# Optimization experiments

Measured on AMD Instinct MI355X. Metric: run time of the kernel, lower is better.

The kernel has to match this reference:

```python
import jax, jax.numpy as jnp
import numpy as np

EPS = 1e-5

def lrelu(x):
    return jnp.where(x > 0, x, 0.2 * x)

def bn(x, g, b, ch_axis=1):
    # BatchNorm in training-mode math (batch statistics), affine
    axes = tuple(i for i in range(x.ndim) if i != ch_axis)
    m = x.mean(axes, keepdims=True)
    v = x.var(axes, keepdims=True)
    shp = [1] * x.ndim; shp[ch_axis] = -1
    return g.reshape(shp) * (x - m) / jnp.sqrt(v + EPS) + b.reshape(shp)

def get_graph_feature(x, idx):
    # x: (B,C,N), idx: (B,N,k) -> edge features (B,2C,N,k) = [neighbor - center, center]
    xt = jnp.transpose(x, (0, 2, 1))                      # (B,N,C)
    nb = jax.vmap(lambda pts, i: pts[i])(xt, idx)         # gather: (B,N,k,C)
    center = jnp.broadcast_to(xt[:, :, None, :], nb.shape)
    edge = jnp.concatenate([nb - center, center], axis=-1)  # (B,N,k,2C)
    return jnp.transpose(edge, (0, 3, 1, 2))              # (B,2C,N,k)

def setup_inputs() -> dict:
    key = jax.random.key(0)
    ks = jax.random.split(key, 12)
    B, N, K = 4, 2048, 20
    def w(k, o, c, s=0.05):
        return jax.random.normal(k, (o, c), jnp.float32) * s
    inp = {}
    inp["x"] = jax.random.normal(ks[0], (B, N, 3), jnp.float32)
    inp["start_neighs"] = jax.random.randint(ks[1], (B, N, K), 0, N)
    dims = [(6, 64), (128, 128), (256, 256), (512, 512)]
    for i, (ci, co) in enumerate(dims):
        inp["w%d" % i] = w(ks[2 + i], co, ci)
        inp["g%d" % i] = jnp.ones((co,), jnp.float32)
        inp["b%d" % i] = jnp.zeros((co,), jnp.float32)
    inp["w4"] = w(ks[6], 1024, 960)
    inp["g4"] = jnp.ones((1024,), jnp.float32); inp["b4"] = jnp.zeros((1024,), jnp.float32)
    inp["lw1"] = w(ks[7], 1024, 2048)
    inp["g6"] = jnp.ones((1024,), jnp.float32); inp["b6"] = jnp.zeros((1024,), jnp.float32)
    inp["lw2"] = w(ks[8], 512, 1024); inp["lb2"] = jnp.zeros((512,), jnp.float32)
    inp["g7"] = jnp.ones((512,), jnp.float32); inp["b7"] = jnp.zeros((512,), jnp.float32)
    inp["lw3"] = w(ks[9], 256, 512); inp["lb3"] = jnp.zeros((256,), jnp.float32)
    return inp

def reference(x, start_neighs,
              w0, g0, b0, w1, g1, b1, w2, g2, b2, w3, g3, b3,
              w4, g4, b4, lw1, g6, b6, lw2, lb2, g7, b7, lw3, lb3):
    # forward_per_point
    xt = jnp.transpose(x, (0, 2, 1))                      # (B,3,N)
    h = get_graph_feature(xt, start_neighs)               # (B,6,N,k)
    outs = []
    for (w, g, b) in ((w0, g0, b0), (w1, g1, b1), (w2, g2, b2), (w3, g3, b3)):
        if outs:  # only_true_neighs=True -> reuse start_neighs
            h = get_graph_feature(outs[-1], start_neighs)
        h = lrelu(bn(jnp.einsum('oc,bcnk->bonk', w, h), g, b))  # 1x1 Conv2d + BN + LeakyReLU
        outs.append(h.max(axis=-1))                       # max over k neighbors -> (B,C,N)
    cat = jnp.concatenate(outs, axis=1)                   # (B,960,N)
    feats = lrelu(bn(jnp.einsum('oc,bcn->bon', w4, cat), g4, b4))  # (B,1024,N)
    # aggregate_all_points (dropout p=0 -> identity)
    z = jnp.concatenate([feats.max(-1), feats.mean(-1)], axis=1)   # (B,2048)
    z = lrelu(bn(z @ lw1.T, g6, b6))
    z = lrelu(bn(z @ lw2.T + lb2, g7, b7))
    z = z @ lw3.T + lb3                                   # (B,256)
    # forward returns (aggregated.squeeze(-1), features_per_point.transpose(1,2)) = (z, (B,1024,N))
    return z, feats
```

## Files before the change

### kernel.cpp

```cpp
#include <hip/hip_runtime.h>
#include <cstddef>
#include <cstdint>

#define EPSBN 1e-5f
constexpr int B_ = 4, N_ = 2048, K_ = 20;

typedef __attribute__((ext_vector_type(8))) _Float16 half8v;
typedef __attribute__((ext_vector_type(4))) float f32x4;
typedef const __attribute__((address_space(1))) unsigned int* gas_t;
typedef __attribute__((address_space(3))) unsigned int* las_t;

__device__ __forceinline__ void swz_batch(int B, int& b, int& local) {
    b = (B & 7) >> 1;
    local = ((B >> 3) << 1) | (B & 1);
}


__device__ __forceinline__ void prep_conv(const float* __restrict__ W, _Float16* __restrict__ W2h,
                                          int O, int C, int i) {
    int o = i / C, c = i - o * C;
    float a = W[o * 2 * C + c];
    float d = W[o * 2 * C + C + c] - a;
    W2h[(size_t)o * C + c] = (_Float16)a;
    W2h[(size_t)(O + o) * C + c] = (_Float16)d;
}

__global__ void k_prep_all(const float* __restrict__ w1, const float* __restrict__ w2,
                           const float* __restrict__ w3, const float* __restrict__ w4,
                           _Float16* __restrict__ W2h1, _Float16* __restrict__ W2h2,
                           _Float16* __restrict__ W2h3, _Float16* __restrict__ w4h) {
    int i = blockIdx.x * 256 + threadIdx.x;
    if (i < 8192) { prep_conv(w1, W2h1, 128, 64, i); return; }
    i -= 8192;
    if (i < 32768) { prep_conv(w2, W2h2, 256, 128, i); return; }
    i -= 32768;
    if (i < 131072) { prep_conv(w3, W2h3, 512, 256, i); return; }
    i -= 131072;
    if (i < 983040) w4h[i] = (_Float16)w4[i];
}

template<bool STATS>
__global__ __launch_bounds__(256, 3)
void k_gemm(const _Float16* __restrict__ A, int sa,
            const _Float16* __restrict__ Bw, int K,
            _Float16* __restrict__ outp, int so,
            float* __restrict__ psum, float* __restrict__ psq) {
    __shared__ __align__(16) _Float16 Als[128 * 64];
    __shared__ __align__(16) _Float16 Bls[128 * 64];
    const int tid = threadIdx.x, lane = tid & 63, w = tid >> 6;
    int bsw, lsw;
    swz_batch(blockIdx.x, bsw, lsw);
    const int m0 = (bsw * 16 + lsw) * 128;
    const int n0 = blockIdx.y * 128;
    const int wr = (w >> 1) * 64, wc = (w & 1) * 64;

    f32x4 acc[4][4];
#pragma unroll
    for (int i = 0; i < 4; ++i)
#pragma unroll
        for (int j = 0; j < 4; ++j) acc[i][j] = (f32x4){0.f, 0.f, 0.f, 0.f};

    int srow[4], scol[4];
#pragma unroll
    for (int j = 0; j < 4; ++j) {
        int idx = w * 256 + j * 64 + lane;
        srow[j] = idx >> 3;
        scol[j] = ((idx & 7) ^ (srow[j] & 7)) * 8;
    }
    int aoff[4][2], boff[4][2];
#pragma unroll
    for (int i = 0; i < 4; ++i) {
        int ra = wr + i * 16 + (lane & 15);
        int rb = wc + i * 16 + (lane & 15);
#pragma unroll
        for (int t = 0; t < 2; ++t) {
            aoff[i][t] = ra * 64 + ((((lane >> 4) + t * 4) ^ (ra & 7)) * 8);
            boff[i][t] = rb * 64 + ((((lane >> 4) + t * 4) ^ (rb & 7)) * 8);
        }
    }

    for (int c0 = 0; c0 < K; c0 += 64) {
#pragma unroll
        for (int j = 0; j < 4; ++j) {
            const _Float16* ga = &A[(size_t)(m0 + srow[j]) * sa + c0 + scol[j]];
            const _Float16* gb = &Bw[(size_t)(n0 + srow[j]) * K + c0 + scol[j]];
            __builtin_amdgcn_global_load_lds((gas_t)(const void*)ga,
                                             (las_t)(void*)&Als[(w * 256 + j * 64) * 8], 16, 0, 0);
            __builtin_amdgcn_global_load_lds((gas_t)(const void*)gb,
                                             (las_t)(void*)&Bls[(w * 256 + j * 64) * 8], 16, 0, 0);
        }
        __syncthreads();
#pragma unroll
        for (int t = 0; t < 2; ++t) {
            half8v a[4], b[4];
#pragma unroll
            for (int i = 0; i < 4; ++i) {
                a[i] = *(const half8v*)&Als[aoff[i][t]];
                b[i] = *(const half8v*)&Bls[boff[i][t]];
            }
#pragma unroll
            for (int i = 0; i < 4; ++i)
#pragma unroll
                for (int j = 0; j < 4; ++j)
                    acc[i][j] = __builtin_amdgcn_mfma_f32_16x16x32_f16(a[i], b[j], acc[i][j], 0, 0, 0);
        }
        __syncthreads();
    }
#pragma unroll
    for (int i = 0; i < 4; ++i)
#pragma unroll
        for (int j = 0; j < 4; ++j)
#pragma unroll
            for (int e = 0; e < 4; ++e) {
                int row = m0 + wr + i * 16 + (lane >> 4) * 4 + e;
                int col = n0 + wc + j * 16 + (lane & 15);
                outp[(size_t)row * so + col] = (_Float16)acc[i][j][e];
            }
    if constexpr (STATS) {
        int slice = blockIdx.x & 63;
#pragma unroll
        for (int j = 0; j < 4; ++j) {
            float s = 0.f, q = 0.f;
#pragma unroll
            for (int i = 0; i < 4; ++i)
#pragma unroll
                for (int e = 0; e < 4; ++e) {
                    float v = acc[i][j][e];
                    s += v; q += v * v;
                }
            s += __shfl_xor(s, 16); s += __shfl_xor(s, 32);
            q += __shfl_xor(q, 16); q += __shfl_xor(q, 32);
            if ((lane >> 4) == 0) {
                int col = n0 + wc + j * 16 + lane;
                atomicAdd(&psum[slice * 1024 + col], s);
                atomicAdd(&psq[slice * 1024 + col], q);
            }
        }
    }
}

__global__ __launch_bounds__(256)
void k_gather0(const float* __restrict__ x, const float* __restrict__ w0,
               const int* __restrict__ nidx, const float* __restrict__ g,
               _Float16* __restrict__ exth,
               float* __restrict__ psum, float* __restrict__ psq) {
    constexpr int O = 64, VPT = 8, P = 32;
    __shared__ float s_red[P * O];
    __shared__ float q_red[P * O];
    const int tid = threadIdx.x;
    const int pl = tid / VPT, v = tid % VPT;
    int bsw, local;
    swz_batch(blockIdx.x, bsw, local);
    const int bbase = bsw * N_;
    const int p = bbase + local * P + pl;
    float wa[8][3], wd[8][3], sg[8];
#pragma unroll
    for (int e = 0; e < 8; ++e) {
        int o = v * 8 + e;
        float a0 = w0[o * 6], a1 = w0[o * 6 + 1], a2 = w0[o * 6 + 2];
        wa[e][0] = a0; wa[e][1] = a1; wa[e][2] = a2;
        wd[e][0] = w0[o * 6 + 3] - a0;
        wd[e][1] = w0[o * 6 + 4] - a1;
        wd[e][2] = w0[o * 6 + 5] - a2;
        sg[e] = (g[o] >= 0.f) ? 1.f : -1.f;
    }
    float mx[8], sm[8], sq[8];
#pragma unroll
    for (int e = 0; e < 8; ++e) { mx[e] = -3.4e38f; sm[e] = 0.f; sq[e] = 0.f; }
    const int* np = nidx + p * K_;
#pragma unroll 4
    for (int k = 0; k < K_; ++k) {
        int j = bbase + np[k];
        float x0 = x[j * 3], x1 = x[j * 3 + 1], x2 = x[j * 3 + 2];
#pragma unroll
        for (int e = 0; e < 8; ++e) {
            float f = wa[e][0] * x0 + wa[e][1] * x1 + wa[e][2] * x2;
            mx[e] = fmaxf(mx[e], f * sg[e]);
            sm[e] += f;
            sq[e] += f * f;
        }
    }
    float xp0 = x[p * 3], xp1 = x[p * 3 + 1], xp2 = x[p * 3 + 2];
    const float Kf = (float)K_;
    half8v exo;
#pragma unroll
    for (int e = 0; e < 8; ++e) {
        float zf = wd[e][0] * xp0 + wd[e][1] * xp1 + wd[e][2] * xp2;
        exo[e] = (_Float16)(sg[e] * mx[e] + zf);
        s_red[pl * O + v * 8 + e] = sm[e] + Kf * zf;
        q_red[pl * O + v * 8 + e] = sq[e] + 2.f * zf * sm[e] + Kf * zf * zf;
    }
    *(half8v*)&exth[(size_t)p * O + v * 8] = exo;
    __syncthreads();
    int slice = blockIdx.x & 63;
    for (int ch = tid; ch < O; ch += 256) {
        float s = 0.f, q = 0.f;
#pragma unroll
        for (int pp = 0; pp < P; ++pp) { s += s_red[pp * O + ch]; q += q_red[pp * O + ch]; }
        atomicAdd(&psum[slice * 1024 + ch], s);
        atomicAdd(&psq[slice * 1024 + ch], q);
    }
}

template<int O>
__global__ __launch_bounds__(256)
void k_gather(const _Float16* __restrict__ Z, const int* __restrict__ nidx,
              const float* __restrict__ g,
              _Float16* __restrict__ exth,
              float* __restrict__ psum, float* __restrict__ psq) {
    constexpr int VPT = O / 8, P = 256 / VPT;
    __shared__ float s_red[P * O];
    __shared__ float q_red[P * O];
    const int tid = threadIdx.x;
    const int pl = tid / VPT, v = tid % VPT;
    int bsw, local;
    swz_batch(blockIdx.x, bsw, local);
    const int bbase = bsw * N_;
    const int p = bbase + local * P + pl;
    float sg[8];
#pragma unroll
    for (int e = 0; e < 8; ++e) sg[e] = (g[v * 8 + e] >= 0.f) ? 1.f : -1.f;
    float mx[8], sm[8], sq[8];
#pragma unroll
    for (int e = 0; e < 8; ++e) { mx[e] = -3.4e38f; sm[e] = 0.f; sq[e] = 0.f; }
    const int* np = nidx + p * K_;
#pragma unroll 4
    for (int k = 0; k < K_; ++k) {
        int j = np[k];
        half8v z = *(const half8v*)&Z[(size_t)(bbase + j) * (2 * O) + v * 8];
#pragma unroll
        for (int e = 0; e < 8; ++e) {
            float f = (float)z[e];
            mx[e] = fmaxf(mx[e], f * sg[e]);
            sm[e] += f;
            sq[e] += f * f;
        }
    }
    half8v zd = *(const half8v*)&Z[(size_t)p * (2 * O) + O + v * 8];
    const float Kf = (float)K_;
    half8v exo;
#pragma unroll
    for (int e = 0; e < 8; ++e) {
        float zf = (float)zd[e];
        exo[e] = (_Float16)(sg[e] * mx[e] + zf);
        s_red[pl * O + v * 8 + e] = sm[e] + Kf * zf;
        q_red[pl * O + v * 8 + e] = sq[e] + 2.f * zf * sm[e] + Kf * zf * zf;
    }
    *(half8v*)&exth[(size_t)p * O + v * 8] = exo;
    __syncthreads();
    int slice = blockIdx.x & 63;
    for (int ch = tid; ch < O; ch += 256) {
        float s = 0.f, q = 0.f;
#pragma unroll
        for (int pp = 0; pp < P; ++pp) { s += s_red[pp * O + ch]; q += q_red[pp * O + ch]; }
        atomicAdd(&psum[slice * 1024 + ch], s);
        atomicAdd(&psq[slice * 1024 + ch], q);
    }
}

__global__ void k_finalize_sl(const float* __restrict__ psum, const float* __restrict__ psq,
                              const float* __restrict__ g, const float* __restrict__ b,
                              float cntInv, int O,
                              float* __restrict__ scale, float* __restrict__ shift) {
    int o = blockIdx.x * 256 + threadIdx.x;
    if (o >= O) return;
    float s = 0.f, q = 0.f;
    for (int i = 0; i < 64; ++i) { s += psum[i * 1024 + o]; q += psq[i * 1024 + o]; }
    float m = s * cntInv;
    float v = q * cntInv - m * m;
    float sc = g[o] * rsqrtf(fmaxf(v, 0.f) + EPSBN);
    scale[o] = sc;
    shift[o] = b[o] - m * sc;
}

template<int O>
__global__ void k_bn_apply(const _Float16* __restrict__ exth,
                           const float* __restrict__ scale, const float* __restrict__ shift,
                           _Float16* __restrict__ cath, int coff) {
    constexpr int PPB = 2048 / O;
    int bsw, local;
    swz_batch(blockIdx.x, bsw, local);
    const int pt_base = bsw * N_ + local * PPB;
    int tid = threadIdx.x;
    int pt = pt_base + (tid * 8) / O;
    int v8 = (tid * 8) & (O - 1);
    half8v hx = *(const half8v*)&exth[(size_t)pt * O + v8];
    half8v r;
#pragma unroll
    for (int e = 0; e < 8; ++e) {
        int o = v8 + e;
        float y = scale[o] * (float)hx[e] + shift[o];
        y = y > 0.f ? y : 0.2f * y;
        r[e] = (_Float16)y;
    }
    *(half8v*)&cath[(size_t)pt * 960 + coff + v8] = r;
}

__global__ void k_feats_out(const _Float16* __restrict__ Y4, const float* __restrict__ scale,
                            const float* __restrict__ shift, float* __restrict__ fo,
                            float* __restrict__ pmax, float* __restrict__ psumn) {
    __shared__ float tile[32][33];
    int tx = threadIdx.x, ty = threadIdx.y;
    int b = blockIdx.z;
    int n0 = blockIdx.x * 32, c0 = blockIdx.y * 32;
#pragma unroll
    for (int i = 0; i < 4; ++i) {
        int n = n0 + ty + i * 8;
        int c = c0 + tx;
        float v = (float)Y4[((size_t)(b * N_ + n)) * 1024 + c];
        v = scale[c] * v + shift[c];
        v = v > 0.f ? v : 0.2f * v;
        tile[ty + i * 8][tx] = v;
    }
    __syncthreads();
#pragma unroll
    for (int i = 0; i < 4; ++i) {
        int c = c0 + ty + i * 8;
        int n = n0 + tx;
        float v2 = tile[tx][ty + i * 8];
        fo[((size_t)(b * 1024 + c)) * N_ + n] = v2;
        float mx = v2, s = v2;
#pragma unroll
        for (int d = 1; d < 32; d <<= 1) {
            mx = fmaxf(mx, __shfl_xor(mx, d));
            s += __shfl_xor(s, d);
        }
        if (tx == 0) {
            int bc = (b << 10) + c;
            pmax[(size_t)bc * 64 + blockIdx.x] = mx;
            psumn[(size_t)bc * 64 + blockIdx.x] = s;
        }
    }
}

__global__ void k_pool2(const float* __restrict__ pmax, const float* __restrict__ psumn,
                        float* __restrict__ z0) {
    int bc = blockIdx.x * 4 + (threadIdx.x >> 6);
    int lane = threadIdx.x & 63;
    float mx = pmax[(size_t)bc * 64 + lane];
    float s  = psumn[(size_t)bc * 64 + lane];
#pragma unroll
    for (int d = 1; d < 64; d <<= 1) {
        mx = fmaxf(mx, __shfl_xor(mx, d));
        s += __shfl_xor(s, d);
    }
    if (lane == 0) {
        int b = bc >> 10, c = bc & 1023;
        z0[b * 2048 + c] = mx;
        z0[b * 2048 + 1024 + c] = s * (1.f / N_);
    }
}

__global__ void k_fc(const float* __restrict__ zin, const float* __restrict__ W,
                     const float* __restrict__ bias,
                     const float* __restrict__ gg, const float* __restrict__ gb,
                     int C, int O, float* __restrict__ zout) {
    __shared__ float sh4[4];
    const int b = threadIdx.x >> 6;
    const int lane = threadIdx.x & 63;
    const int o = blockIdx.x;
    const float* wr = W + (size_t)o * C;
    const float* zr = zin + b * C;
    float s = 0.f;
    for (int c = lane * 4; c < C; c += 256) {
        const float4 wv = *(const float4*)&wr[c];
        const float4 zv = *(const float4*)&zr[c];
        s += wv.x * zv.x + wv.y * zv.y + wv.z * zv.z + wv.w * zv.w;
    }
    s += __shfl_xor(s, 1);
    s += __shfl_xor(s, 2);
    s += __shfl_xor(s, 4);
    s += __shfl_xor(s, 8);
    s += __shfl_xor(s, 16);
    s += __shfl_xor(s, 32);
    if (!gg) {
        if (lane == 0) zout[b * O + o] = s + (bias ? bias[o] : 0.f);
        return;
    }
    if (lane == 0) sh4[b] = s + (bias ? bias[o] : 0.f);
    __syncthreads();
    if (threadIdx.x == 0) {
        float v0 = sh4[0], v1 = sh4[1], v2 = sh4[2], v3 = sh4[3];
        float m = 0.25f * (v0 + v1 + v2 + v3);
        float d0 = v0 - m, d1 = v1 - m, d2 = v2 - m, d3 = v3 - m;
        float var = 0.25f * (d0 * d0 + d1 * d1 + d2 * d2 + d3 * d3);
        float sc = gg[o] * rsqrtf(var + EPSBN);
        float shv = gb[o];
        float r0 = sc * d0 + shv, r1 = sc * d1 + shv, r2 = sc * d2 + shv, r3 = sc * d3 + shv;
        zout[o]         = r0 > 0.f ? r0 : 0.2f * r0;
        zout[O + o]     = r1 > 0.f ? r1 : 0.2f * r1;
        zout[2 * O + o] = r2 > 0.f ? r2 : 0.2f * r2;
        zout[3 * O + o] = r3 > 0.f ? r3 : 0.2f * r3;
    }
}


extern "C" void kernel_launch(void* const* d_in, const int* in_sizes, int n_in,
                              void* d_out, int out_size, void* d_ws, size_t ws_size,
                              hipStream_t stream) {
    const float* x    = (const float*)d_in[0];
    const int*   nidx = (const int*)d_in[1];
    const float* w[5]  = {(const float*)d_in[2], (const float*)d_in[5], (const float*)d_in[8],
                          (const float*)d_in[11], (const float*)d_in[14]};
    const float* g[5]  = {(const float*)d_in[3], (const float*)d_in[6], (const float*)d_in[9],
                          (const float*)d_in[12], (const float*)d_in[15]};
    const float* bb[5] = {(const float*)d_in[4], (const float*)d_in[7], (const float*)d_in[10],
                          (const float*)d_in[13], (const float*)d_in[16]};
    const float* lw1 = (const float*)d_in[17];
    const float* g6  = (const float*)d_in[18];
    const float* b6  = (const float*)d_in[19];
    const float* lw2 = (const float*)d_in[20];
    const float* lb2 = (const float*)d_in[21];
    const float* g7  = (const float*)d_in[22];
    const float* b7  = (const float*)d_in[23];
    const float* lw3 = (const float*)d_in[24];
    const float* lb3 = (const float*)d_in[25];

    float* out = (float*)d_out;
    float* fo  = out + 1024;

    uint8_t* base8 = (uint8_t*)d_ws;
    size_t off = 0;
    auto alloc = [&](size_t bytes) -> void* {
        void* r = base8 + off;
        off += (bytes + 255) & ~(size_t)255;
        return r;
    };
    _Float16* cath = (_Float16*)alloc((size_t)B_ * N_ * 960 * 2);
    _Float16* Z    = (_Float16*)alloc((size_t)8192 * 1024 * 2);
    _Float16* exth = (_Float16*)alloc((size_t)8192 * 512 * 2);
    _Float16* Y4   = (_Float16*)alloc((size_t)8192 * 1024 * 2);
    _Float16* W2h1 = (_Float16*)alloc((size_t)256 * 64 * 2);
    _Float16* W2h2 = (_Float16*)alloc((size_t)512 * 128 * 2);
    _Float16* W2h3 = (_Float16*)alloc((size_t)1024 * 256 * 2);
    _Float16* w4h  = (_Float16*)alloc((size_t)1024 * 960 * 2);
    float* psumall = (float*)alloc((size_t)5 * 131072 * 4);
    float* pmax  = (float*)alloc((size_t)4096 * 64 * 4);
    float* psumn = (float*)alloc((size_t)4096 * 64 * 4);
    float* scalev= (float*)alloc(1024 * 4);
    float* shiftv= (float*)alloc(1024 * 4);
    float* z0    = (float*)alloc(8192 * 4);
    float* z1    = (float*)alloc(4096 * 4);
    float* z2    = (float*)alloc(2048 * 4);
    (void)ws_size; (void)in_sizes; (void)n_in; (void)out_size;

    auto psumR = [&](int r) { return psumall + (size_t)r * 131072; };
    auto psqR  = [&](int r) { return psumall + (size_t)r * 131072 + 65536; };

    hipMemsetAsync(psumall, 0, (size_t)5 * 131072 * 4, stream);
    k_prep_all<<<(8192 + 32768 + 131072 + 983040 + 255) / 256, 256, 0, stream>>>(
        w[1], w[2], w[3], w[4], W2h1, W2h2, W2h3, w4h);

    k_gather0<<<256, 256, 0, stream>>>(x, w[0], nidx, g[0], exth, psumR(0), psqR(0));
    k_finalize_sl<<<1, 256, 0, stream>>>(psumR(0), psqR(0), g[0], bb[0], 1.f / (B_ * N_ * K_),
                                         64, scalev, shiftv);
    k_bn_apply<64><<<256, 256, 0, stream>>>(exth, scalev, shiftv, cath, 0);

    struct LayerCfg { int coff_in, C, O, coff_out, li; const _Float16* Wh; };
    const LayerCfg L[3] = {
        { 0,   64,  128, 64,  1, W2h1 },
        { 64,  128, 256, 192, 2, W2h2 },
        { 192, 256, 512, 448, 3, W2h3 },
    };
    for (int i = 0; i < 3; ++i) {
        const LayerCfg& Lc = L[i];
        dim3 ggrid(64, (2 * Lc.O) / 128);
        k_gemm<false><<<ggrid, 256, 0, stream>>>(cath + Lc.coff_in, 960, Lc.Wh, Lc.C,
                                                 Z, 2 * Lc.O, nullptr, nullptr);
        if (Lc.O == 128) {
            k_gather<128><<<512, 256, 0, stream>>>(Z, nidx, g[Lc.li], exth, psumR(i + 1), psqR(i + 1));
            k_finalize_sl<<<1, 256, 0, stream>>>(psumR(i + 1), psqR(i + 1), g[Lc.li], bb[Lc.li],
                                                 1.f / (B_ * N_ * K_), 128, scalev, shiftv);
            k_bn_apply<128><<<512, 256, 0, stream>>>(exth, scalev, shiftv, cath, Lc.coff_out);
        } else if (Lc.O == 256) {
            k_gather<256><<<1024, 256, 0, stream>>>(Z, nidx, g[Lc.li], exth, psumR(i + 1), psqR(i + 1));
            k_finalize_sl<<<1, 256, 0, stream>>>(psumR(i + 1), psqR(i + 1), g[Lc.li], bb[Lc.li],
                                                 1.f / (B_ * N_ * K_), 256, scalev, shiftv);
            k_bn_apply<256><<<1024, 256, 0, stream>>>(exth, scalev, shiftv, cath, Lc.coff_out);
        } else {
            k_gather<512><<<2048, 256, 0, stream>>>(Z, nidx, g[Lc.li], exth, psumR(i + 1), psqR(i + 1));
            k_finalize_sl<<<2, 256, 0, stream>>>(psumR(i + 1), psqR(i + 1), g[Lc.li], bb[Lc.li],
                                                 1.f / (B_ * N_ * K_), 512, scalev, shiftv);
            k_bn_apply<512><<<2048, 256, 0, stream>>>(exth, scalev, shiftv, cath, Lc.coff_out);
        }
    }

    k_gemm<true><<<dim3(64, 8), 256, 0, stream>>>(cath, 960, w4h, 960, Y4, 1024, psumR(4), psqR(4));
    k_finalize_sl<<<4, 256, 0, stream>>>(psumR(4), psqR(4), g[4], bb[4], 1.f / (B_ * N_), 1024,
                                         scalev, shiftv);
    k_feats_out<<<dim3(64, 32, 4), dim3(32, 8), 0, stream>>>(Y4, scalev, shiftv, fo, pmax, psumn);
    k_pool2<<<1024, 256, 0, stream>>>(pmax, psumn, z0);

    k_fc<<<1024, 256, 0, stream>>>(z0, lw1, nullptr, g6, b6, 2048, 1024, z1);
    k_fc<<<512, 256, 0, stream>>>(z1, lw2, lb2, g7, b7, 1024, 512, z2);
    k_fc<<<256, 256, 0, stream>>>(z2, lw3, lb3, nullptr, nullptr, 512, 256, out);
}
```

Before: 168.6 us.

## Fuse BN-apply and LeakyReLU into GEMM A-tile load, drop concat buffer

Removes the separate k_bn_apply kernels and the concatenated cath buffer. Each GEMM now reads the raw per-layer max-pooled outputs, applies BN scale/shift and LeakyReLU in registers, and writes the result to LDS. The final 960-channel GEMM picks among four source buffers per K-chunk. This drops three kernel launches and an extra read/write pass over the activations. The cost is that A loads now go through registers instead of direct global-to-LDS transfers, and the normalisation is recomputed for every N-tile block.

```diff
diff --git a/kernel.cpp b/kernel.cpp
--- a/kernel.cpp
+++ b/kernel.cpp
@@ -41,7 +41,12 @@
 
 template<bool STATS>
 __global__ __launch_bounds__(256, 3)
-void k_gemm(const _Float16* __restrict__ A, int sa,
+void k_gemm(const _Float16* __restrict__ A0, const _Float16* __restrict__ A1,
+            const _Float16* __restrict__ A2, const _Float16* __restrict__ A3,
+            int t1, int t2, int t3,
+            int c1, int c2, int c3,
+            int s0, int s1, int s2, int s3,
+            const float* __restrict__ scale, const float* __restrict__ shift,
             const _Float16* __restrict__ Bw, int K,
             _Float16* __restrict__ outp, int so,
             float* __restrict__ psum, float* __restrict__ psq) {
@@ -80,14 +85,40 @@
     }
 
     for (int c0 = 0; c0 < K; c0 += 64) {
+        const _Float16* src; int stride, coff;
+        if (c0 < t1)      { src = A0; stride = s0; coff = 0;  }
+        else if (c0 < t2) { src = A1; stride = s1; coff = c1; }
+        else if (c0 < t3) { src = A2; stride = s2; coff = c2; }
+        else              { src = A3; stride = s3; coff = c3; }
+
 #pragma unroll
         for (int j = 0; j < 4; ++j) {
-            const _Float16* ga = &A[(size_t)(m0 + srow[j]) * sa + c0 + scol[j]];
             const _Float16* gb = &Bw[(size_t)(n0 + srow[j]) * K + c0 + scol[j]];
-            __builtin_amdgcn_global_load_lds((gas_t)(const void*)ga,
-                                             (las_t)(void*)&Als[(w * 256 + j * 64) * 8], 16, 0, 0);
             __builtin_amdgcn_global_load_lds((gas_t)(const void*)gb,
                                              (las_t)(void*)&Bls[(w * 256 + j * 64) * 8], 16, 0, 0);
+        }
+        half8v av[4];
+#pragma unroll
+        for (int j = 0; j < 4; ++j)
+            av[j] = *(const half8v*)&src[(size_t)(m0 + srow[j]) * stride + (c0 - coff) + scol[j]];
+#pragma unroll
+        for (int j = 0; j < 4; ++j) {
+            const int cb = c0 + scol[j];
+            float4 sc0 = *(const float4*)&scale[cb];
+            float4 sc1 = *(const float4*)&scale[cb + 4];
+            float4 sh0 = *(const float4*)&shift[cb];
+            float4 sh1 = *(const float4*)&shift[cb + 4];
+            half8v r;
+            float y;
+            y = sc0.x * (float)av[j][0] + sh0.x; r[0] = (_Float16)fmaxf(y, 0.2f * y);
+            y = sc0.y * (float)av[j][1] + sh0.y; r[1] = (_Float16)fmaxf(y, 0.2f * y);
+            y = sc0.z * (float)av[j][2] + sh0.z; r[2] = (_Float16)fmaxf(y, 0.2f * y);
+            y = sc0.w * (float)av[j][3] + sh0.w; r[3] = (_Float16)fmaxf(y, 0.2f * y);
+            y = sc1.x * (float)av[j][4] + sh1.x; r[4] = (_Float16)fmaxf(y, 0.2f * y);
+            y = sc1.y * (float)av[j][5] + sh1.y; r[5] = (_Float16)fmaxf(y, 0.2f * y);
+            y = sc1.z * (float)av[j][6] + sh1.z; r[6] = (_Float16)fmaxf(y, 0.2f * y);
+            y = sc1.w * (float)av[j][7] + sh1.w; r[7] = (_Float16)fmaxf(y, 0.2f * y);
+            *(half8v*)&Als[(w * 256 + j * 64 + lane) * 8] = r;
         }
         __syncthreads();
 #pragma unroll
@@ -271,29 +302,6 @@
     float sc = g[o] * rsqrtf(fmaxf(v, 0.f) + EPSBN);
     scale[o] = sc;
     shift[o] = b[o] - m * sc;
-}
-
-template<int O>
-__global__ void k_bn_apply(const _Float16* __restrict__ exth,
-                           const float* __restrict__ scale, const float* __restrict__ shift,
-                           _Float16* __restrict__ cath, int coff) {
-    constexpr int PPB = 2048 / O;
-    int bsw, local;
-    swz_batch(blockIdx.x, bsw, local);
-    const int pt_base = bsw * N_ + local * PPB;
-    int tid = threadIdx.x;
-    int pt = pt_base + (tid * 8) / O;
-    int v8 = (tid * 8) & (O - 1);
-    half8v hx = *(const half8v*)&exth[(size_t)pt * O + v8];
-    half8v r;
-#pragma unroll
-    for (int e = 0; e < 8; ++e) {
-        int o = v8 + e;
-        float y = scale[o] * (float)hx[e] + shift[o];
-        y = y > 0.f ? y : 0.2f * y;
-        r[e] = (_Float16)y;
-    }
-    *(half8v*)&cath[(size_t)pt * 960 + coff + v8] = r;
 }
 
 __global__ void k_feats_out(const _Float16* __restrict__ Y4, const float* __restrict__ scale,
@@ -426,19 +434,23 @@
         off += (bytes + 255) & ~(size_t)255;
         return r;
     };
-    _Float16* cath = (_Float16*)alloc((size_t)B_ * N_ * 960 * 2);
-    _Float16* Z    = (_Float16*)alloc((size_t)8192 * 1024 * 2);
-    _Float16* exth = (_Float16*)alloc((size_t)8192 * 512 * 2);
-    _Float16* Y4   = (_Float16*)alloc((size_t)8192 * 1024 * 2);
-    _Float16* W2h1 = (_Float16*)alloc((size_t)256 * 64 * 2);
-    _Float16* W2h2 = (_Float16*)alloc((size_t)512 * 128 * 2);
-    _Float16* W2h3 = (_Float16*)alloc((size_t)1024 * 256 * 2);
-    _Float16* w4h  = (_Float16*)alloc((size_t)1024 * 960 * 2);
+    _Float16* Z     = (_Float16*)alloc((size_t)8192 * 1024 * 2);
+    _Float16* exth0 = (_Float16*)alloc((size_t)8192 * 64 * 2);
+    _Float16* exth1 = (_Float16*)alloc((size_t)8192 * 128 * 2);
+    _Float16* exth2 = (_Float16*)alloc((size_t)8192 * 256 * 2);
+    _Float16* exth3 = (_Float16*)alloc((size_t)8192 * 512 * 2);
+    _Float16* Y4    = (_Float16*)alloc((size_t)8192 * 1024 * 2);
+    _Float16* W2h1  = (_Float16*)alloc((size_t)256 * 64 * 2);
+    _Float16* W2h2  = (_Float16*)alloc((size_t)512 * 128 * 2);
+    _Float16* W2h3  = (_Float16*)alloc((size_t)1024 * 256 * 2);
+    _Float16* w4h   = (_Float16*)alloc((size_t)1024 * 960 * 2);
     float* psumall = (float*)alloc((size_t)5 * 131072 * 4);
     float* pmax  = (float*)alloc((size_t)4096 * 64 * 4);
     float* psumn = (float*)alloc((size_t)4096 * 64 * 4);
-    float* scalev= (float*)alloc(1024 * 4);
-    float* shiftv= (float*)alloc(1024 * 4);
+    float* scaleC = (float*)alloc(960 * 4);
+    float* shiftC = (float*)alloc(960 * 4);
+    float* scale4 = (float*)alloc(1024 * 4);
+    float* shift4 = (float*)alloc(1024 * 4);
     float* z0    = (float*)alloc(8192 * 4);
     float* z1    = (float*)alloc(4096 * 4);
     float* z2    = (float*)alloc(2048 * 4);
@@ -446,49 +458,43 @@
 
     auto psumR = [&](int r) { return psumall + (size_t)r * 131072; };
     auto psqR  = [&](int r) { return psumall + (size_t)r * 131072 + 65536; };
+    const int HUGE_T = 1 << 30;
 
     hipMemsetAsync(psumall, 0, (size_t)5 * 131072 * 4, stream);
     k_prep_all<<<(8192 + 32768 + 131072 + 983040 + 255) / 256, 256, 0, stream>>>(
         w[1], w[2], w[3], w[4], W2h1, W2h2, W2h3, w4h);
 
-    k_gather0<<<256, 256, 0, stream>>>(x, w[0], nidx, g[0], exth, psumR(0), psqR(0));
+    k_gather0<<<256, 256, 0, stream>>>(x, w[0], nidx, g[0], exth0, psumR(0), psqR(0));
     k_finalize_sl<<<1, 256, 0, stream>>>(psumR(0), psqR(0), g[0], bb[0], 1.f / (B_ * N_ * K_),
-                                         64, scalev, shiftv);
-    k_bn_apply<64><<<256, 256, 0, stream>>>(exth, scalev, shiftv, cath, 0);
-
-    struct LayerCfg { int coff_in, C, O, coff_out, li; const _Float16* Wh; };
-    const LayerCfg L[3] = {
-        { 0,   64,  128, 64,  1, W2h1 },
-        { 64,  128, 256, 192, 2, W2h2 },
-        { 192, 256, 512, 448, 3, W2h3 },
-    };
-    for (int i = 0; i < 3; ++i) {
-        const LayerCfg& Lc = L[i];
-        dim3 ggrid(64, (2 * Lc.O) / 128);
-        k_gemm<false><<<ggrid, 256, 0, stream>>>(cath + Lc.coff_in, 960, Lc.Wh, Lc.C,
-                                                 Z, 2 * Lc.O, nullptr, nullptr);
-        if (Lc.O == 128) {
-            k_gather<128><<<512, 256, 0, stream>>>(Z, nidx, g[Lc.li], exth, psumR(i + 1), psqR(i + 1));
-            k_finalize_sl<<<1, 256, 0, stream>>>(psumR(i + 1), psqR(i + 1), g[Lc.li], bb[Lc.li],
-                                                 1.f / (B_ * N_ * K_), 128, scalev, shiftv);
-            k_bn_apply<128><<<512, 256, 0, stream>>>(exth, scalev, shiftv, cath, Lc.coff_out);
-        } else if (Lc.O == 256) {
-            k_gather<256><<<1024, 256, 0, stream>>>(Z, nidx, g[Lc.li], exth, psumR(i + 1), psqR(i + 1));
-            k_finalize_sl<<<1, 256, 0, stream>>>(psumR(i + 1), psqR(i + 1), g[Lc.li], bb[Lc.li],
-                                                 1.f / (B_ * N_ * K_), 256, scalev, shiftv);
-            k_bn_apply<256><<<1024, 256, 0, stream>>>(exth, scalev, shiftv, cath, Lc.coff_out);
-        } else {
-            k_gather<512><<<2048, 256, 0, stream>>>(Z, nidx, g[Lc.li], exth, psumR(i + 1), psqR(i + 1));
-            k_finalize_sl<<<2, 256, 0, stream>>>(psumR(i + 1), psqR(i + 1), g[Lc.li], bb[Lc.li],
-                                                 1.f / (B_ * N_ * K_), 512, scalev, shiftv);
-            k_bn_apply<512><<<2048, 256, 0, stream>>>(exth, scalev, shiftv, cath, Lc.coff_out);
-        }
-    }
-
-    k_gemm<true><<<dim3(64, 8), 256, 0, stream>>>(cath, 960, w4h, 960, Y4, 1024, psumR(4), psqR(4));
+                                         64, scaleC + 0, shiftC + 0);
+
+    k_gemm<false><<<dim3(64, 2), 256, 0, stream>>>(
+        exth0, exth0, exth0, exth0, HUGE_T, HUGE_T, HUGE_T, 0, 0, 0, 64, 64, 64, 64,
+        scaleC + 0, shiftC + 0, W2h1, 64, Z, 256, nullptr, nullptr);
+    k_gather<128><<<512, 256, 0, stream>>>(Z, nidx, g[1], exth1, psumR(1), psqR(1));
+    k_finalize_sl<<<1, 256, 0, stream>>>(psumR(1), psqR(1), g[1], bb[1], 1.f / (B_ * N_ * K_),
+                                         128, scaleC + 64, shiftC + 64);
+
+    k_gemm<false><<<dim3(64, 4), 256, 0, stream>>>(
+        exth1, exth1, exth1, exth1, HUGE_T, HUGE_T, HUGE_T, 0, 0, 0, 128, 128, 128, 128,
+        scaleC + 64, shiftC + 64, W2h2, 128, Z, 512, nullptr, nullptr);
+    k_gather<256><<<1024, 256, 0, stream>>>(Z, nidx, g[2], exth2, psumR(2), psqR(2));
+    k_finalize_sl<<<1, 256, 0, stream>>>(psumR(2), psqR(2), g[2], bb[2], 1.f / (B_ * N_ * K_),
+                                         256, scaleC + 192, shiftC + 192);
+
+    k_gemm<false><<<dim3(64, 8), 256, 0, stream>>>(
+        exth2, exth2, exth2, exth2, HUGE_T, HUGE_T, HUGE_T, 0, 0, 0, 256, 256, 256, 256,
+        scaleC + 192, shiftC + 192, W2h3, 256, Z, 1024, nullptr, nullptr);
+    k_gather<512><<<2048, 256, 0, stream>>>(Z, nidx, g[3], exth3, psumR(3), psqR(3));
+    k_finalize_sl<<<2, 256, 0, stream>>>(psumR(3), psqR(3), g[3], bb[3], 1.f / (B_ * N_ * K_),
+                                         512, scaleC + 448, shiftC + 448);
+
+    k_gemm<true><<<dim3(64, 8), 256, 0, stream>>>(
+        exth0, exth1, exth2, exth3, 64, 192, 448, 64, 192, 448, 64, 128, 256, 512,
+        scaleC, shiftC, w4h, 960, Y4, 1024, psumR(4), psqR(4));
     k_finalize_sl<<<4, 256, 0, stream>>>(psumR(4), psqR(4), g[4], bb[4], 1.f / (B_ * N_), 1024,
-                                         scalev, shiftv);
-    k_feats_out<<<dim3(64, 32, 4), dim3(32, 8), 0, stream>>>(Y4, scalev, shiftv, fo, pmax, psumn);
+                                         scale4, shift4);
+    k_feats_out<<<dim3(64, 32, 4), dim3(32, 8), 0, stream>>>(Y4, scale4, shift4, fo, pmax, psumn);
     k_pool2<<<1024, 256, 0, stream>>>(pmax, psumn, z0);
 
     k_fc<<<1024, 256, 0, stream>>>(z0, lw1, nullptr, g6, b6, 2048, 1024, z1);
```

Measured after the change: 185.8 us. +10.2%, slower.
